# Performance work log

Measured on AMD Instinct MI355X. Metric: run time of the kernel, lower is better.

## Reference

```python
import jax, jax.numpy as jnp
import numpy as np

N, E = 32768, 524288
MUL = 32        # multiplicity of 0e and 1o in hidden irreps
N_ATTR = 4      # node attr scalars (species one-hot)
N_RAD = 8       # radial basis size
FC_H = 64       # radial MLP hidden width
AVG_NEIGH = 16.0
INV3 = 1.0 / np.sqrt(3.0)  # w3j(1,1,0) contraction coefficient


def setup_inputs() -> dict:
    key = jax.random.key(0)
    ks = jax.random.split(key, 16)
    p = lambda k, s: jax.random.normal(k, s, dtype=jnp.float32)
    return {
        "node_feats": p(ks[0], (N, MUL + 3 * MUL)),
        "node_attrs": jax.random.uniform(ks[1], (N, N_ATTR), dtype=jnp.float32),
        "edge_feats": p(ks[2], (E, N_RAD)),
        "edge_attrs": p(ks[3], (E, 4)),
        "W1s": p(ks[4], (MUL, MUL)),
        "W1v": p(ks[5], (MUL, MUL)),
        "Wf1": p(ks[6], (N_RAD, FC_H)),
        "Wf2": p(ks[7], (FC_H, FC_H)),
        "Wf3": p(ks[8], (FC_H, 4 * MUL)),
        "W2s": p(ks[9], (2 * MUL, 2 * MUL)),
        "W2v": p(ks[10], (2 * MUL, MUL)),
        "Wsc_s": p(ks[11], (MUL, N_ATTR, 2 * MUL)),
        "Wsc_v": p(ks[12], (MUL, N_ATTR, MUL)),
        "edge_index": jax.random.randint(ks[13], (2, E), 0, N),
    }


def reference(node_feats, node_attrs, edge_feats, edge_attrs,
              W1s, W1v, Wf1, Wf2, Wf3, W2s, W2v, Wsc_s, Wsc_v, edge_index):
    silu = jax.nn.silu
    sender, receiver = edge_index[0], edge_index[1]
    xs0 = node_feats[:, :MUL]                      # [N, MUL]   0e scalars
    xv0 = node_feats[:, MUL:].reshape(-1, MUL, 3)  # [N, MUL, 3] 1o vectors

    # linear_1 (irrep-wise, e3nn fan-in normalization)
    xs = (xs0 @ W1s) / np.sqrt(MUL)
    xv = jnp.einsum('nui,uv->nvi', xv0, W1v) / np.sqrt(MUL)

    # radial MLP -> per-edge tensor-product weights
    h = silu((edge_feats @ Wf1) / np.sqrt(N_RAD))
    h = silu((h @ Wf2) / np.sqrt(FC_H))
    w = (h @ Wf3) / np.sqrt(FC_H)                  # [E, 4*MUL]
    w0, w1, w2, w3 = jnp.split(w, 4, axis=1)       # [E, MUL] each

    sh0 = edge_attrs[:, :1]                        # [E, 1]  l=0
    sh1 = edge_attrs[:, 1:4]                       # [E, 3]  l=1
    xs_e = xs[sender]                              # [E, MUL]
    xv_e = xv[sender]                              # [E, MUL, 3]

    # per-edge 'uvu' tensor product paths (only paths landing in 0e/1o kept)
    m_s0 = w0 * xs_e * sh0                                      # 0e x 0e -> 0e
    m_s1 = w3 * jnp.einsum('eui,ei->eu', xv_e, sh1) * INV3      # 1o x 1o -> 0e
    m_v0 = (w1 * xs_e)[:, :, None] * sh1[:, None, :]            # 0e x 1o -> 1o
    m_v1 = (w2 * sh0)[:, :, None] * xv_e                        # 1o x 0e -> 1o

    msg_s = jnp.concatenate([m_s0, m_s1], axis=1)               # [E, 2*MUL]
    msg_v = jnp.concatenate([m_v0, m_v1], axis=1)               # [E, 2*MUL, 3]

    # scatter-add message passing, normalized by avg num neighbours
    agg_s = jax.ops.segment_sum(msg_s, receiver, num_segments=N) / AVG_NEIGH
    agg_v = jax.ops.segment_sum(msg_v, receiver, num_segments=N) / AVG_NEIGH

    # linear_2 to conv output irreps (2*MUL x 0e + MUL x 1o)
    out_s = (agg_s @ W2s) / np.sqrt(2 * MUL)                    # [N, 2*MUL]
    out_v = jnp.einsum('nui,uv->nvi', agg_v, W2v) / np.sqrt(2 * MUL)

    # self connection: FullyConnectedTensorProduct(x_in, node_attrs)
    norm_sc = 1.0 / np.sqrt(MUL * N_ATTR)
    out_s = out_s + jnp.einsum('nu,na,uaw->nw', xs0, node_attrs, Wsc_s) * norm_sc
    out_v = out_v + jnp.einsum('nui,na,uaw->nwi', xv0, node_attrs, Wsc_v) * norm_sc

    # Gate nonlinearity: act(scalars) ++ act(gates) * gated vectors
    scalars = silu(out_s[:, :MUL])
    gates = silu(out_s[:, MUL:])
    gated = out_v * gates[:, :, None]
    new_feats = jnp.concatenate([scalars, gated.reshape(-1, 3 * MUL)], axis=1)

    # resnet add (irreps_layer_out == interaction_irreps_in)
    return node_feats + new_feats
```

## Files before the change

### kernel.cpp

```cpp
#include <hip/hip_runtime.h>
#include <hip/hip_bf16.h>

#define NN 32768
#define NE 524288

typedef __attribute__((ext_vector_type(8))) short short8v;
typedef __attribute__((ext_vector_type(4))) short short4v;
typedef __attribute__((ext_vector_type(4))) float f32x4;

__device__ __forceinline__ float silu_f(float x){ return x * (1.0f/(1.0f+__expf(-x))); }
__device__ __forceinline__ float bf2f(unsigned short u){ return __uint_as_float(((unsigned)u)<<16); }
__device__ __forceinline__ unsigned short f2bf(float f){
  __hip_bfloat16 b = __float2bfloat16(f);
  return __builtin_bit_cast(unsigned short, b);
}
__device__ __forceinline__ unsigned pk2(float lo, float hi){
  return (unsigned)f2bf(lo) | ((unsigned)f2bf(hi) << 16);
}

#define S32 0.17677669529663687f
#define S8  0.35355339059327373f
#define S64 0.125f
#define R16 0.0625f
#define NSC 0.08838834764831845f
#define INV3F 0.5773502691896258f

__global__ void k_zero(int* __restrict__ deg){
  deg[blockIdx.x*256 + threadIdx.x] = 0;
}

__global__ void k_hist(const int* __restrict__ eidx, int* __restrict__ deg){
  int e = blockIdx.x*256 + threadIdx.x;
  int r = eidx[NE + e];
  atomicAdd(&deg[r], 1);
}

__global__ void __launch_bounds__(1024) k_scan(const int* __restrict__ deg,
    int* __restrict__ row_start, int* __restrict__ cursor){
  __shared__ int lds[1024];
  int t = threadIdx.x;
  int4 v[8];
  const int4* dg = reinterpret_cast<const int4*>(deg) + t*8;
  int s = 0;
  #pragma unroll
  for (int j=0;j<8;j++){ v[j] = dg[j]; s += v[j].x+v[j].y+v[j].z+v[j].w; }
  lds[t] = s; __syncthreads();
  for (int off=1; off<1024; off<<=1){
    int q = (t>=off)? lds[t-off] : 0; __syncthreads();
    lds[t] += q; __syncthreads();
  }
  int run = (t==0)?0:lds[t-1];
  int4* rs = reinterpret_cast<int4*>(row_start) + t*8;
  int4* cu = reinterpret_cast<int4*>(cursor) + t*8;
  #pragma unroll
  for (int j=0;j<8;j++){
    int4 o;
    o.x = run; run += v[j].x;
    o.y = run; run += v[j].y;
    o.z = run; run += v[j].z;
    o.w = run; run += v[j].w;
    rs[j] = o; cu[j] = o;
  }
  if (t==1023) row_start[NN] = run;
}

__global__ void k_scatter(const int* __restrict__ eidx, int* __restrict__ cursor,
                          int2* __restrict__ csre){
  int e = blockIdx.x*256 + threadIdx.x;
  int r = eidx[NE + e];
  int s = eidx[e];
  int pos = atomicAdd(&cursor[r], 1);
  csre[pos] = make_int2(e, s);
}

#define XT_ITERS 16
__global__ void __launch_bounds__(256) k_xt(const float* __restrict__ nf,
    const float* __restrict__ W1s, const float* __restrict__ W1v,
    float* __restrict__ xtp2){
  __shared__ float rowbuf[256];
  int t = threadIdx.x;
  int c = t & 127, u = c >> 2, comp = c & 3;
  int node = t >> 7;
  const float* W = (comp==0) ? W1s : W1v;
  float wreg[32];
  #pragma unroll
  for (int k=0;k<32;k++) wreg[k] = W[k*32 + u];
  int soff = node*128 + (comp==0 ? 0 : 32 + (comp-1));
  int stride = (comp==0) ? 1 : 3;
  int base = blockIdx.x * (2*XT_ITERS);
  #pragma unroll 1
  for (int it=0; it<XT_ITERS; it++){
    int n0 = base + it*2;
    __syncthreads();
    rowbuf[t] = nf[(size_t)n0*128 + t];
    __syncthreads();
    float acc = 0.f;
    #pragma unroll
    for (int k=0;k<32;k++) acc += rowbuf[soff + k*stride] * wreg[k];
    xtp2[(size_t)(n0+node)*128 + c] = acc * S32;
  }
}

__global__ void k_wprep(const float* __restrict__ Wf1, const float* __restrict__ Wf2,
                        const float* __restrict__ Wf3,
                        const float* __restrict__ W2s, const float* __restrict__ W2v,
                        const float* __restrict__ Wsc_s, const float* __restrict__ Wsc_v,
                        short* __restrict__ wfrag, short* __restrict__ wfe){
  int f = blockIdx.x;
  int l = threadIdx.x;
  int c = l & 15, g = l >> 4;
  short8v pk;
  if (f < 28){
    #pragma unroll
    for (int j=0;j<8;j++){
      int k = ((j&4) ? 16 : 0) + g*4 + (j&3);
      float val;
      if (f < 4){
        int m = f;
        val = (k < 8) ? Wf1[k*64 + m*16 + c] : 0.f;
      } else if (f < 12){
        int idx = f-4, m = idx>>1, kk = idx&1;
        val = Wf2[(kk*32+k)*64 + m*16 + c];
      } else {
        int idx = f-12, m = idx>>1, kk = idx&1;
        val = Wf3[(kk*32+k)*128 + m*16 + c];
      }
      pk[j] = (short)f2bf(val);
    }
    reinterpret_cast<short8v*>(wfrag)[f*64 + l] = pk;
  } else {
    int fe = f - 28, kb = fe/6, p = fe%6;
    #pragma unroll
    for (int j=0;j<8;j++){
      int k = kb*32 + ((j&4) ? 16 : 0) + g*4 + (j&3);
      float val;
      if (p < 4){
        int col = p*16 + c;
        val = (k < 64) ? W2s[k*64 + col]*S64 : Wsc_s[(k-64)*64 + col]*NSC;
      } else {
        int col = (p-4)*16 + c;
        val = (k < 64) ? W2v[k*32 + col]*S64 : Wsc_v[(k-64)*32 + col]*NSC;
      }
      pk[j] = (short)f2bf(val);
    }
    reinterpret_cast<short8v*>(wfe)[fe*64 + l] = pk;
  }
}

__global__ void __launch_bounds__(256) k_mlp2(const float* __restrict__ ef,
    const short* __restrict__ wfrag, unsigned* __restrict__ wpair){
  __shared__ unsigned sb[4][16][68];
  int lane = threadIdx.x & 63;
  int wv = threadIdx.x >> 6;
  int wid = blockIdx.x*4 + wv;
  int e_l = lane & 15, g = lane >> 4;
  const short8v* wf = reinterpret_cast<const short8v*>(wfrag);

  #pragma unroll 1
  for (int s=0; s<2; s++){
    int tile = wid*2 + s;
    short8v bx = {};
    if (lane < 32){
      const float4 xv = *reinterpret_cast<const float4*>(
          ef + (size_t)(tile*16 + e_l)*8 + g*4);
      bx[0]=(short)f2bf(xv.x); bx[1]=(short)f2bf(xv.y);
      bx[2]=(short)f2bf(xv.z); bx[3]=(short)f2bf(xv.w);
    }
    f32x4 a1[4];
    #pragma unroll
    for (int m=0;m<4;m++){
      f32x4 z = {};
      a1[m] = __builtin_amdgcn_mfma_f32_16x16x32_bf16(wf[m*64+lane], bx, z, 0,0,0);
    }
    short8v b2[2];
    #pragma unroll
    for (int m=0;m<4;m++)
      #pragma unroll
      for (int r=0;r<4;r++)
        b2[m>>1][(m&1)*4 + r] = (short)f2bf(silu_f(a1[m][r]*S8));
    f32x4 a2[4] = {};
    #pragma unroll
    for (int kk=0;kk<2;kk++)
      #pragma unroll
      for (int m=0;m<4;m++)
        a2[m] = __builtin_amdgcn_mfma_f32_16x16x32_bf16(wf[(4+2*m+kk)*64+lane], b2[kk], a2[m], 0,0,0);
    short8v b3[2];
    #pragma unroll
    for (int m=0;m<4;m++)
      #pragma unroll
      for (int r=0;r<4;r++)
        b3[m>>1][(m&1)*4 + r] = (short)f2bf(silu_f(a2[m][r]*S64));
    f32x4 a3[8] = {};
    #pragma unroll
    for (int kk=0;kk<2;kk++)
      #pragma unroll
      for (int m=0;m<8;m++)
        a3[m] = __builtin_amdgcn_mfma_f32_16x16x32_bf16(wf[(12+2*m+kk)*64+lane], b3[kk], a3[m], 0,0,0);
    #pragma unroll
    for (int mm=0; mm<2; mm++){
      uint4 o;
      o.x = pk2(a3[mm][0]*S64, a3[mm+2][0]*S64);
      o.y = pk2(a3[mm][1]*S64, a3[mm+2][1]*S64);
      o.z = pk2(a3[mm][2]*S64, a3[mm+2][2]*S64);
      o.w = pk2(a3[mm][3]*S64, a3[mm+2][3]*S64);
      *reinterpret_cast<uint4*>(&sb[wv][e_l][mm*16 + g*4]) = o;
      uint4 o2;
      o2.x = pk2(a3[6+mm][0]*S64*INV3F, a3[4+mm][0]*S64);
      o2.y = pk2(a3[6+mm][1]*S64*INV3F, a3[4+mm][1]*S64);
      o2.z = pk2(a3[6+mm][2]*S64*INV3F, a3[4+mm][2]*S64);
      o2.w = pk2(a3[6+mm][3]*S64*INV3F, a3[4+mm][3]*S64);
      *reinterpret_cast<uint4*>(&sb[wv][e_l][32 + mm*16 + g*4]) = o2;
    }
    __syncthreads();
    unsigned* gd = wpair + (size_t)tile*1024;
    #pragma unroll
    for (int q=0;q<4;q++){
      uint4 v = *reinterpret_cast<uint4*>(&sb[wv][lane>>2][(lane&3)*16 + q*4]);
      *reinterpret_cast<uint4*>(gd + lane*16 + q*4) = v;
    }
    __syncthreads();
  }
}

__global__ void __launch_bounds__(256) k_recv(
    const float* __restrict__ ea, const int* __restrict__ row_start,
    const int2* __restrict__ csre, const unsigned* __restrict__ wpair,
    const float* __restrict__ xtp2, unsigned* __restrict__ agg){
  __shared__ float L[4][256];
  int wb = threadIdx.x >> 6;
  int lane = threadIdx.x & 63;
  int nl = wb >> 1, w = wb & 1;
  int n = blockIdx.x*2 + nl;
  int u = lane & 31;
  bool h1 = lane >= 32;

  int row = row_start[n], end = row_start[n+1];
  int mid = (row + end + 1) >> 1;
  int lo = w ? mid : row;
  int hi = w ? end : mid;

  float a0=0.f, a1=0.f, a2=0.f, a3=0.f;

  auto body = [&](int2 es){
    int e  = __builtin_amdgcn_readfirstlane(es.x);
    int sn = __builtin_amdgcn_readfirstlane(es.y);
    float4 sh = *reinterpret_cast<const float4*>(ea + (size_t)e*4);
    unsigned wp = wpair[(size_t)e*64 + lane];
    float4 q = *reinterpret_cast<const float4*>(xtp2 + (size_t)sn*128 + u*4);
    float wA = bf2f((unsigned short)(wp & 0xffffu));
    float wB = bf2f((unsigned short)(wp >> 16));
    float x0 = h1 ? q.y : q.x;
    float x1 = h1 ? q.z : q.x;
    float x2 = h1 ? q.w : q.x;
    float c0 = h1 ? sh.y : sh.x;
    float c1 = h1 ? sh.z : 0.f;
    float c2 = h1 ? sh.w : 0.f;
    a0 += wA*(x0*c0 + x1*c1 + x2*c2);
    float g0 = wB*(h1 ? sh.x : sh.y);
    float g1 = wB*(h1 ? sh.x : sh.z);
    float g2 = wB*(h1 ? sh.x : sh.w);
    a1 += g0*x0; a2 += g1*x1; a3 += g2*x2;
  };

  int idx = lo;
  for (; idx+4 <= hi; idx += 4){
    int2 e0 = csre[idx], e1 = csre[idx+1], e2 = csre[idx+2], e3 = csre[idx+3];
    body(e0); body(e1); body(e2); body(e3);
  }
  for (; idx < hi; ++idx) body(csre[idx]);

  float* P = L[wb];
  P[lane] = a0; P[64+lane] = a1; P[128+lane] = a2; P[192+lane] = a3;
  __syncthreads();

  int t = threadIdx.x;
  int nl2 = t >> 7, cp = t & 127;
  float v0 = (L[nl2*2][2*cp  ] + L[nl2*2+1][2*cp  ]) * R16;
  float v1 = (L[nl2*2][2*cp+1] + L[nl2*2+1][2*cp+1]) * R16;
  agg[(size_t)(blockIdx.x*2 + nl2)*128 + cp] = pk2(v0, v1);
}

__global__ void __launch_bounds__(256) k_epi(
    const float* __restrict__ nf, const float* __restrict__ na,
    const unsigned short* __restrict__ agg, const short* __restrict__ wfe,
    float* __restrict__ out){
  __shared__ float L[4][16][168];
  int wv = threadIdx.x >> 6, lane = threadIdx.x & 63;
  int tile = blockIdx.x*4 + wv;
  int e = lane & 15, g = lane >> 4;
  int n = tile*16 + e;
  const short8v* WE = reinterpret_cast<const short8v*>(wfe);
  const unsigned short* ag = agg + (size_t)n*256;
  const float* nfr = nf + (size_t)n*128;
  float4 nav = *reinterpret_cast<const float4*>(na + (size_t)n*4);

  f32x4 as0={},as1={},as2={},as3={};
  f32x4 av00={},av01={},av10={},av11={},av20={},av21={};

  #pragma unroll
  for (int kb=0; kb<6; kb++){
    short8v bs, bv0, bv1, bv2;
    if (kb < 2){
      int k0 = kb*32 + g*4;
      #pragma unroll
      for (int i=0;i<4;i++){
        short4v qa = *reinterpret_cast<const short4v*>(ag + i*64 + k0);
        short4v qb = *reinterpret_cast<const short4v*>(ag + i*64 + k0 + 16);
        short8v b;
        b[0]=qa[0]; b[1]=qa[1]; b[2]=qa[2]; b[3]=qa[3];
        b[4]=qb[0]; b[5]=qb[1]; b[6]=qb[2]; b[7]=qb[3];
        if (i==0) bs = b; else if (i==1) bv0 = b; else if (i==2) bv1 = b; else bv2 = b;
      }
    } else {
      int u0 = (kb-2)*8 + g;
      float x0 = nfr[u0], x1 = nfr[u0+4];
      bs[0]=(short)f2bf(x0*nav.x); bs[1]=(short)f2bf(x0*nav.y);
      bs[2]=(short)f2bf(x0*nav.z); bs[3]=(short)f2bf(x0*nav.w);
      bs[4]=(short)f2bf(x1*nav.x); bs[5]=(short)f2bf(x1*nav.y);
      bs[6]=(short)f2bf(x1*nav.z); bs[7]=(short)f2bf(x1*nav.w);
      #pragma unroll
      for (int i=0;i<3;i++){
        float y0 = nfr[32 + u0*3 + i], y1 = nfr[32 + (u0+4)*3 + i];
        short8v b;
        b[0]=(short)f2bf(y0*nav.x); b[1]=(short)f2bf(y0*nav.y);
        b[2]=(short)f2bf(y0*nav.z); b[3]=(short)f2bf(y0*nav.w);
        b[4]=(short)f2bf(y1*nav.x); b[5]=(short)f2bf(y1*nav.y);
        b[6]=(short)f2bf(y1*nav.z); b[7]=(short)f2bf(y1*nav.w);
        if (i==0) bv0 = b; else if (i==1) bv1 = b; else bv2 = b;
      }
    }
    as0 = __builtin_amdgcn_mfma_f32_16x16x32_bf16(WE[(kb*6+0)*64+lane], bs, as0, 0,0,0);
    as1 = __builtin_amdgcn_mfma_f32_16x16x32_bf16(WE[(kb*6+1)*64+lane], bs, as1, 0,0,0);
    as2 = __builtin_amdgcn_mfma_f32_16x16x32_bf16(WE[(kb*6+2)*64+lane], bs, as2, 0,0,0);
    as3 = __builtin_amdgcn_mfma_f32_16x16x32_bf16(WE[(kb*6+3)*64+lane], bs, as3, 0,0,0);
    av00 = __builtin_amdgcn_mfma_f32_16x16x32_bf16(WE[(kb*6+4)*64+lane], bv0, av00, 0,0,0);
    av01 = __builtin_amdgcn_mfma_f32_16x16x32_bf16(WE[(kb*6+5)*64+lane], bv0, av01, 0,0,0);
    av10 = __builtin_amdgcn_mfma_f32_16x16x32_bf16(WE[(kb*6+4)*64+lane], bv1, av10, 0,0,0);
    av11 = __builtin_amdgcn_mfma_f32_16x16x32_bf16(WE[(kb*6+5)*64+lane], bv1, av11, 0,0,0);
    av20 = __builtin_amdgcn_mfma_f32_16x16x32_bf16(WE[(kb*6+4)*64+lane], bv2, av20, 0,0,0);
    av21 = __builtin_amdgcn_mfma_f32_16x16x32_bf16(WE[(kb*6+5)*64+lane], bv2, av21, 0,0,0);
  }

  float (*Lw)[168] = L[wv];
  #pragma unroll
  for (int r=0;r<4;r++){
    Lw[e][ 0 + g*4 + r] = silu_f(as0[r]);
    Lw[e][16 + g*4 + r] = silu_f(as1[r]);
    Lw[e][32 + g*4 + r] = silu_f(as2[r]);
    Lw[e][48 + g*4 + r] = silu_f(as3[r]);
    Lw[e][64 + (     g*4 + r)*3 + 0] = av00[r];
    Lw[e][64 + (16 + g*4 + r)*3 + 0] = av01[r];
    Lw[e][64 + (     g*4 + r)*3 + 1] = av10[r];
    Lw[e][64 + (16 + g*4 + r)*3 + 1] = av11[r];
    Lw[e][64 + (     g*4 + r)*3 + 2] = av20[r];
    Lw[e][64 + (16 + g*4 + r)*3 + 2] = av21[r];
  }
  __syncthreads();

  if (g == 0){
    #pragma unroll
    for (int c=0;c<32;c+=4){
      float4 nv = *reinterpret_cast<const float4*>(nfr + c);
      float4 o;
      o.x = nv.x + Lw[e][c  ];
      o.y = nv.y + Lw[e][c+1];
      o.z = nv.z + Lw[e][c+2];
      o.w = nv.w + Lw[e][c+3];
      *reinterpret_cast<float4*>(out + (size_t)n*128 + c) = o;
    }
  } else {
    int q0 = (g-1)*32;
    #pragma unroll
    for (int q=q0; q<q0+32; q+=4){
      float4 nv = *reinterpret_cast<const float4*>(nfr + 32 + q);
      float4 o;
      o.x = nv.x + Lw[e][64+q+0]*Lw[e][32+(q+0)/3];
      o.y = nv.y + Lw[e][64+q+1]*Lw[e][32+(q+1)/3];
      o.z = nv.z + Lw[e][64+q+2]*Lw[e][32+(q+2)/3];
      o.w = nv.w + Lw[e][64+q+3]*Lw[e][32+(q+3)/3];
      *reinterpret_cast<float4*>(out + (size_t)n*128 + 32 + q) = o;
    }
  }
}

extern "C" void kernel_launch(void* const* d_in, const int* in_sizes, int n_in,
                              void* d_out, int out_size, void* d_ws, size_t ws_size,
                              hipStream_t stream) {
  const float* nf    = (const float*)d_in[0];
  const float* na    = (const float*)d_in[1];
  const float* ef    = (const float*)d_in[2];
  const float* ea    = (const float*)d_in[3];
  const float* W1s   = (const float*)d_in[4];
  const float* W1v   = (const float*)d_in[5];
  const float* Wf1   = (const float*)d_in[6];
  const float* Wf2   = (const float*)d_in[7];
  const float* Wf3   = (const float*)d_in[8];
  const float* W2s   = (const float*)d_in[9];
  const float* W2v   = (const float*)d_in[10];
  const float* Wsc_s = (const float*)d_in[11];
  const float* Wsc_v = (const float*)d_in[12];
  const int*   eidx  = (const int*)d_in[13];
  float* out = (float*)d_out;

  char* ws = (char*)d_ws;
  size_t off = 0;
  auto alloc = [&](size_t bytes)->void*{
    void* p = ws + off; off += (bytes + 255) & ~(size_t)255; return p;
  };
  float*    xtp2      = (float*)alloc((size_t)NN*128*4);
  unsigned* wpair     = (unsigned*)alloc((size_t)NE*64*4);
  unsigned* agg       = (unsigned*)alloc((size_t)NN*256*2);
  int*      deg       = (int*)alloc((size_t)NN*4);
  int*      row_start = (int*)alloc((size_t)(NN+16)*4);
  int*      cursor    = (int*)alloc((size_t)NN*4);
  int2*     csre      = (int2*)alloc((size_t)NE*8);
  short*    wfrag     = (short*)alloc((size_t)28*64*8*2);
  short*    wfe       = (short*)alloc((size_t)36*64*8*2);
  if (off > ws_size) return;

  k_zero   <<<NN/256, 256, 0, stream>>>(deg);
  k_hist   <<<NE/256, 256, 0, stream>>>(eidx, deg);
  k_scan   <<<1, 1024, 0, stream>>>(deg, row_start, cursor);
  k_scatter<<<NE/256, 256, 0, stream>>>(eidx, cursor, csre);
  k_xt     <<<NN/(2*XT_ITERS), 256, 0, stream>>>(nf, W1s, W1v, xtp2);
  k_wprep  <<<64, 64, 0, stream>>>(Wf1, Wf2, Wf3, W2s, W2v, Wsc_s, Wsc_v, wfrag, wfe);
  k_mlp2   <<<4096, 256, 0, stream>>>(ef, wfrag, wpair);
  k_recv   <<<NN/2, 256, 0, stream>>>(ea, row_start, csre, wpair, xtp2,
                                      (unsigned*)agg);
  k_epi    <<<512, 256, 0, stream>>>(nf, na, (const unsigned short*)agg, wfe, out);
}
```

Before: 247.9 us.

## Compute radial MLP in receiver-sorted edge order and batch gathers in recv

The radial MLP now reads edges through the CSR permutation, so per-edge weights and spherical harmonics are written in receiver-sorted order. k_recv can then stream them contiguously instead of gathering them by edge id. The recv loop also issues eight edges' loads before computing, to raise memory-level parallelism. MLP scale factors are folded into the prepacked weights, the LDS staging and syncs in k_mlp2 are removed, and csre is split into eperm and sperm arrays. In exchange, the MLP's reads of edge_feats become scattered gathers, there is an extra shp buffer to write, and direct stores from MFMA fragments may coalesce less well.

```diff
diff --git a/kernel.cpp b/kernel.cpp
--- a/kernel.cpp
+++ b/kernel.cpp
@@ -65,12 +65,13 @@
 }
 
 __global__ void k_scatter(const int* __restrict__ eidx, int* __restrict__ cursor,
-                          int2* __restrict__ csre){
+                          int* __restrict__ eperm, int* __restrict__ sperm){
   int e = blockIdx.x*256 + threadIdx.x;
   int r = eidx[NE + e];
   int s = eidx[e];
   int pos = atomicAdd(&cursor[r], 1);
-  csre[pos] = make_int2(e, s);
+  eperm[pos] = e;
+  sperm[pos] = s;
 }
 
 #define XT_ITERS 16
@@ -117,13 +118,14 @@
       float val;
       if (f < 4){
         int m = f;
-        val = (k < 8) ? Wf1[k*64 + m*16 + c] : 0.f;
+        val = (k < 8) ? Wf1[k*64 + m*16 + c]*S8 : 0.f;
       } else if (f < 12){
         int idx = f-4, m = idx>>1, kk = idx&1;
-        val = Wf2[(kk*32+k)*64 + m*16 + c];
+        val = Wf2[(kk*32+k)*64 + m*16 + c]*S64;
       } else {
         int idx = f-12, m = idx>>1, kk = idx&1;
-        val = Wf3[(kk*32+k)*128 + m*16 + c];
+        val = Wf3[(kk*32+k)*128 + m*16 + c]*S64;
+        if (m >= 6) val *= INV3F;
       }
       pk[j] = (short)f2bf(val);
     }
@@ -148,83 +150,76 @@
 }
 
 __global__ void __launch_bounds__(256) k_mlp2(const float* __restrict__ ef,
-    const short* __restrict__ wfrag, unsigned* __restrict__ wpair){
-  __shared__ unsigned sb[4][16][68];
+    const float* __restrict__ ea, const int* __restrict__ eperm,
+    const short* __restrict__ wfrag, unsigned* __restrict__ wpair,
+    float4* __restrict__ shp){
   int lane = threadIdx.x & 63;
   int wv = threadIdx.x >> 6;
-  int wid = blockIdx.x*4 + wv;
+  int tile = blockIdx.x*4 + wv;
   int e_l = lane & 15, g = lane >> 4;
   const short8v* wf = reinterpret_cast<const short8v*>(wfrag);
 
-  #pragma unroll 1
-  for (int s=0; s<2; s++){
-    int tile = wid*2 + s;
-    short8v bx = {};
-    if (lane < 32){
-      const float4 xv = *reinterpret_cast<const float4*>(
-          ef + (size_t)(tile*16 + e_l)*8 + g*4);
-      bx[0]=(short)f2bf(xv.x); bx[1]=(short)f2bf(xv.y);
-      bx[2]=(short)f2bf(xv.z); bx[3]=(short)f2bf(xv.w);
-    }
-    f32x4 a1[4];
-    #pragma unroll
-    for (int m=0;m<4;m++){
-      f32x4 z = {};
-      a1[m] = __builtin_amdgcn_mfma_f32_16x16x32_bf16(wf[m*64+lane], bx, z, 0,0,0);
-    }
-    short8v b2[2];
+  int pos = tile*16 + e_l;
+  int e = eperm[pos];
+  if (lane < 16) shp[pos] = *reinterpret_cast<const float4*>(ea + (size_t)e*4);
+
+  short8v bx = {};
+  if (lane < 32){
+    const float4 xv = *reinterpret_cast<const float4*>(ef + (size_t)e*8 + g*4);
+    bx[0]=(short)f2bf(xv.x); bx[1]=(short)f2bf(xv.y);
+    bx[2]=(short)f2bf(xv.z); bx[3]=(short)f2bf(xv.w);
+  }
+  f32x4 a1[4];
+  #pragma unroll
+  for (int m=0;m<4;m++){
+    f32x4 z = {};
+    a1[m] = __builtin_amdgcn_mfma_f32_16x16x32_bf16(wf[m*64+lane], bx, z, 0,0,0);
+  }
+  short8v b2[2];
+  #pragma unroll
+  for (int m=0;m<4;m++)
+    #pragma unroll
+    for (int r=0;r<4;r++)
+      b2[m>>1][(m&1)*4 + r] = (short)f2bf(silu_f(a1[m][r]));
+  f32x4 a2[4] = {};
+  #pragma unroll
+  for (int kk=0;kk<2;kk++)
     #pragma unroll
     for (int m=0;m<4;m++)
-      #pragma unroll
-      for (int r=0;r<4;r++)
-        b2[m>>1][(m&1)*4 + r] = (short)f2bf(silu_f(a1[m][r]*S8));
-    f32x4 a2[4] = {};
-    #pragma unroll
-    for (int kk=0;kk<2;kk++)
-      #pragma unroll
-      for (int m=0;m<4;m++)
-        a2[m] = __builtin_amdgcn_mfma_f32_16x16x32_bf16(wf[(4+2*m+kk)*64+lane], b2[kk], a2[m], 0,0,0);
-    short8v b3[2];
-    #pragma unroll
-    for (int m=0;m<4;m++)
-      #pragma unroll
-      for (int r=0;r<4;r++)
-        b3[m>>1][(m&1)*4 + r] = (short)f2bf(silu_f(a2[m][r]*S64));
-    f32x4 a3[8] = {};
-    #pragma unroll
-    for (int kk=0;kk<2;kk++)
-      #pragma unroll
-      for (int m=0;m<8;m++)
-        a3[m] = __builtin_amdgcn_mfma_f32_16x16x32_bf16(wf[(12+2*m+kk)*64+lane], b3[kk], a3[m], 0,0,0);
-    #pragma unroll
-    for (int mm=0; mm<2; mm++){
-      uint4 o;
-      o.x = pk2(a3[mm][0]*S64, a3[mm+2][0]*S64);
-      o.y = pk2(a3[mm][1]*S64, a3[mm+2][1]*S64);
-      o.z = pk2(a3[mm][2]*S64, a3[mm+2][2]*S64);
-      o.w = pk2(a3[mm][3]*S64, a3[mm+2][3]*S64);
-      *reinterpret_cast<uint4*>(&sb[wv][e_l][mm*16 + g*4]) = o;
-      uint4 o2;
-      o2.x = pk2(a3[6+mm][0]*S64*INV3F, a3[4+mm][0]*S64);
-      o2.y = pk2(a3[6+mm][1]*S64*INV3F, a3[4+mm][1]*S64);
-      o2.z = pk2(a3[6+mm][2]*S64*INV3F, a3[4+mm][2]*S64);
-      o2.w = pk2(a3[6+mm][3]*S64*INV3F, a3[4+mm][3]*S64);
-      *reinterpret_cast<uint4*>(&sb[wv][e_l][32 + mm*16 + g*4]) = o2;
-    }
-    __syncthreads();
-    unsigned* gd = wpair + (size_t)tile*1024;
-    #pragma unroll
-    for (int q=0;q<4;q++){
-      uint4 v = *reinterpret_cast<uint4*>(&sb[wv][lane>>2][(lane&3)*16 + q*4]);
-      *reinterpret_cast<uint4*>(gd + lane*16 + q*4) = v;
-    }
-    __syncthreads();
+      a2[m] = __builtin_amdgcn_mfma_f32_16x16x32_bf16(wf[(4+2*m+kk)*64+lane], b2[kk], a2[m], 0,0,0);
+  short8v b3[2];
+  #pragma unroll
+  for (int m=0;m<4;m++)
+    #pragma unroll
+    for (int r=0;r<4;r++)
+      b3[m>>1][(m&1)*4 + r] = (short)f2bf(silu_f(a2[m][r]));
+  f32x4 a3[8] = {};
+  #pragma unroll
+  for (int kk=0;kk<2;kk++)
+    #pragma unroll
+    for (int m=0;m<8;m++)
+      a3[m] = __builtin_amdgcn_mfma_f32_16x16x32_bf16(wf[(12+2*m+kk)*64+lane], b3[kk], a3[m], 0,0,0);
+  unsigned* dst = wpair + (size_t)tile*1024 + e_l*64;
+  #pragma unroll
+  for (int mm=0; mm<2; mm++){
+    uint4 o;
+    o.x = pk2(a3[mm][0], a3[mm+2][0]);
+    o.y = pk2(a3[mm][1], a3[mm+2][1]);
+    o.z = pk2(a3[mm][2], a3[mm+2][2]);
+    o.w = pk2(a3[mm][3], a3[mm+2][3]);
+    *reinterpret_cast<uint4*>(dst + mm*16 + g*4) = o;
+    uint4 o2;
+    o2.x = pk2(a3[6+mm][0], a3[4+mm][0]);
+    o2.y = pk2(a3[6+mm][1], a3[4+mm][1]);
+    o2.z = pk2(a3[6+mm][2], a3[4+mm][2]);
+    o2.w = pk2(a3[6+mm][3], a3[4+mm][3]);
+    *reinterpret_cast<uint4*>(dst + 32 + mm*16 + g*4) = o2;
   }
 }
 
 __global__ void __launch_bounds__(256) k_recv(
-    const float* __restrict__ ea, const int* __restrict__ row_start,
-    const int2* __restrict__ csre, const unsigned* __restrict__ wpair,
+    const float4* __restrict__ shp, const int* __restrict__ row_start,
+    const int* __restrict__ sperm, const unsigned* __restrict__ wpair,
     const float* __restrict__ xtp2, unsigned* __restrict__ agg){
   __shared__ float L[4][256];
   int wb = threadIdx.x >> 6;
@@ -241,33 +236,66 @@
 
   float a0=0.f, a1=0.f, a2=0.f, a3=0.f;
 
-  auto body = [&](int2 es){
-    int e  = __builtin_amdgcn_readfirstlane(es.x);
-    int sn = __builtin_amdgcn_readfirstlane(es.y);
-    float4 sh = *reinterpret_cast<const float4*>(ea + (size_t)e*4);
-    unsigned wp = wpair[(size_t)e*64 + lane];
-    float4 q = *reinterpret_cast<const float4*>(xtp2 + (size_t)sn*128 + u*4);
-    float wA = bf2f((unsigned short)(wp & 0xffffu));
-    float wB = bf2f((unsigned short)(wp >> 16));
-    float x0 = h1 ? q.y : q.x;
-    float x1 = h1 ? q.z : q.x;
-    float x2 = h1 ? q.w : q.x;
-    float c0 = h1 ? sh.y : sh.x;
-    float c1 = h1 ? sh.z : 0.f;
-    float c2 = h1 ? sh.w : 0.f;
-    a0 += wA*(x0*c0 + x1*c1 + x2*c2);
-    float g0 = wB*(h1 ? sh.x : sh.y);
-    float g1 = wB*(h1 ? sh.x : sh.z);
-    float g2 = wB*(h1 ? sh.x : sh.w);
-    a1 += g0*x0; a2 += g1*x1; a3 += g2*x2;
-  };
+#define EDGE_BODY(WP, SH, Q)                                         \
+  {                                                                  \
+    float wA = bf2f((unsigned short)((WP) & 0xffffu));               \
+    float wB = bf2f((unsigned short)((WP) >> 16));                   \
+    float x0 = h1 ? (Q).y : (Q).x;                                   \
+    float x1 = h1 ? (Q).z : (Q).x;                                   \
+    float x2 = h1 ? (Q).w : (Q).x;                                   \
+    float c0 = h1 ? (SH).y : (SH).x;                                 \
+    float c1 = h1 ? (SH).z : 0.f;                                    \
+    float c2 = h1 ? (SH).w : 0.f;                                    \
+    a0 += wA*(x0*c0 + x1*c1 + x2*c2);                                \
+    float g0 = wB*(h1 ? (SH).x : (SH).y);                            \
+    float g1 = wB*(h1 ? (SH).x : (SH).z);                            \
+    float g2 = wB*(h1 ? (SH).x : (SH).w);                            \
+    a1 += g0*x0; a2 += g1*x1; a3 += g2*x2;                           \
+  }
 
   int idx = lo;
+  for (; idx+8 <= hi; idx += 8){
+    int sn[8]; unsigned wp[8]; float4 sh[8]; float4 q[8];
+    #pragma unroll
+    for (int j=0;j<8;j++) sn[j] = sperm[idx+j];
+    #pragma unroll
+    for (int j=0;j<8;j++){
+      wp[j] = wpair[(size_t)(idx+j)*64 + lane];
+      sh[j] = shp[idx+j];
+    }
+    #pragma unroll
+    for (int j=0;j<8;j++){
+      int sb = __builtin_amdgcn_readfirstlane(sn[j]);
+      q[j] = *reinterpret_cast<const float4*>(xtp2 + (size_t)sb*128 + u*4);
+    }
+    #pragma unroll
+    for (int j=0;j<8;j++) EDGE_BODY(wp[j], sh[j], q[j]);
+  }
   for (; idx+4 <= hi; idx += 4){
-    int2 e0 = csre[idx], e1 = csre[idx+1], e2 = csre[idx+2], e3 = csre[idx+3];
-    body(e0); body(e1); body(e2); body(e3);
-  }
-  for (; idx < hi; ++idx) body(csre[idx]);
+    int sn[4]; unsigned wp[4]; float4 sh[4]; float4 q[4];
+    #pragma unroll
+    for (int j=0;j<4;j++) sn[j] = sperm[idx+j];
+    #pragma unroll
+    for (int j=0;j<4;j++){
+      wp[j] = wpair[(size_t)(idx+j)*64 + lane];
+      sh[j] = shp[idx+j];
+    }
+    #pragma unroll
+    for (int j=0;j<4;j++){
+      int sb = __builtin_amdgcn_readfirstlane(sn[j]);
+      q[j] = *reinterpret_cast<const float4*>(xtp2 + (size_t)sb*128 + u*4);
+    }
+    #pragma unroll
+    for (int j=0;j<4;j++) EDGE_BODY(wp[j], sh[j], q[j]);
+  }
+  for (; idx < hi; ++idx){
+    int sb = __builtin_amdgcn_readfirstlane(sperm[idx]);
+    unsigned wp = wpair[(size_t)idx*64 + lane];
+    float4 sh = shp[idx];
+    float4 q = *reinterpret_cast<const float4*>(xtp2 + (size_t)sb*128 + u*4);
+    EDGE_BODY(wp, sh, q);
+  }
+#undef EDGE_BODY
 
   float* P = L[wb];
   P[lane] = a0; P[64+lane] = a1; P[128+lane] = a2; P[192+lane] = a3;
@@ -410,10 +438,12 @@
   float*    xtp2      = (float*)alloc((size_t)NN*128*4);
   unsigned* wpair     = (unsigned*)alloc((size_t)NE*64*4);
   unsigned* agg       = (unsigned*)alloc((size_t)NN*256*2);
+  float4*   shp       = (float4*)alloc((size_t)NE*16);
   int*      deg       = (int*)alloc((size_t)NN*4);
   int*      row_start = (int*)alloc((size_t)(NN+16)*4);
   int*      cursor    = (int*)alloc((size_t)NN*4);
-  int2*     csre      = (int2*)alloc((size_t)NE*8);
+  int*      eperm     = (int*)alloc((size_t)NE*4);
+  int*      sperm     = (int*)alloc((size_t)NE*4);
   short*    wfrag     = (short*)alloc((size_t)28*64*8*2);
   short*    wfe       = (short*)alloc((size_t)36*64*8*2);
   if (off > ws_size) return;
@@ -421,11 +451,11 @@
   k_zero   <<<NN/256, 256, 0, stream>>>(deg);
   k_hist   <<<NE/256, 256, 0, stream>>>(eidx, deg);
   k_scan   <<<1, 1024, 0, stream>>>(deg, row_start, cursor);
-  k_scatter<<<NE/256, 256, 0, stream>>>(eidx, cursor, csre);
+  k_scatter<<<NE/256, 256, 0, stream>>>(eidx, cursor, eperm, sperm);
   k_xt     <<<NN/(2*XT_ITERS), 256, 0, stream>>>(nf, W1s, W1v, xtp2);
   k_wprep  <<<64, 64, 0, stream>>>(Wf1, Wf2, Wf3, W2s, W2v, Wsc_s, Wsc_v, wfrag, wfe);
-  k_mlp2   <<<4096, 256, 0, stream>>>(ef, wfrag, wpair);
-  k_recv   <<<NN/2, 256, 0, stream>>>(ea, row_start, csre, wpair, xtp2,
+  k_mlp2   <<<8192, 256, 0, stream>>>(ef, ea, eperm, wfrag, wpair, shp);
+  k_recv   <<<NN/2, 256, 0, stream>>>(shp, row_start, sperm, wpair, xtp2,
                                       (unsigned*)agg);
   k_epi    <<<512, 256, 0, stream>>>(nf, na, (const unsigned short*)agg, wfe, out);
 }
```

Result: slower. 356.1 us (+43.6%).
